# Optimization experiments

Hardware: AMD Instinct MI355X
Metric: run time of the kernel (lower is better)

The kernel has to match this reference:

```python
import jax, jax.numpy as jnp
import numpy as np

B, D, O = 512, 256, 256
H = [512, 1024, 1024]

def _linear_params(key, fan_in, fan_out):
    kw, kb = jax.random.split(key)
    bound = 1.0 / np.sqrt(fan_in)
    W = jax.random.uniform(kw, (fan_out, fan_in), jnp.float32, -bound, bound)
    b = jax.random.uniform(kb, (fan_out,), jnp.float32, -bound, bound)
    return W, b

def setup_inputs() -> dict:
    key = jax.random.key(0)
    ks = jax.random.split(key, 7)
    input_values = jax.random.normal(ks[0], (B, D), jnp.float32)
    nan_flag = jax.random.uniform(ks[1], (B, D), jnp.float32)
    W_in, b_in = _linear_params(ks[2], D, H[0])          # input_layer: nan_flag_dim -> H[0]
    W_h1, b_h1 = _linear_params(ks[3], H[0], H[1])        # hidden layer 1
    W_h2, b_h2 = _linear_params(ks[4], H[1], H[2])        # hidden layer 2
    W_d, b_d = _linear_params(ks[5], H[2], D * O)         # output_branch_dense
    W_b, b_b = _linear_params(ks[6], H[2], O)             # output_branch_bias
    return {"input_values": input_values, "nan_flag": nan_flag, "training": False,
            "W_in": W_in, "b_in": b_in, "W_h1": W_h1, "b_h1": b_h1,
            "W_h2": W_h2, "b_h2": b_h2, "W_d": W_d, "b_d": b_d,
            "W_b": W_b, "b_b": b_b}

def reference(input_values, nan_flag, training, W_in, b_in, W_h1, b_h1, W_h2, b_h2, W_d, b_d, W_b, b_b):
    # training=False: dropout is identity, sample_missing branch skipped (default False)
    x = jax.nn.relu(nan_flag @ W_in.T + b_in)
    x = jax.nn.relu(x @ W_h1.T + b_h1)
    x = jax.nn.relu(x @ W_h2.T + b_h2)
    # per-sample compensation weights [B, D, O] and bias [B, O]
    comp_w = (x @ W_d.T + b_d).reshape(B, D, O)
    comp_b = x @ W_b.T + b_b
    # baddbmm: [B,1,D] @ [B,D,O] + [B,1,O] -> squeeze -> [B,O]
    out = comp_b + jnp.einsum('bd,bdo->bo', input_values, comp_w)
    return out
```

## Files before the change

kernel.cpp:

```cpp
#include <hip/hip_runtime.h>
#include <hip/hip_bf16.h>

#define B_  512
#define D_  256
#define O_  256
#define H2_ 1024

typedef __attribute__((ext_vector_type(4))) float  f32x4;
typedef __attribute__((ext_vector_type(8))) short  short8;
typedef __attribute__((ext_vector_type(4))) short  short4v;

union S8u { short4v v; unsigned u[2]; };

__device__ __forceinline__ unsigned f32_bf16(float x) {
  unsigned u = __builtin_bit_cast(unsigned, x);
  return (u + 0x7fffu + ((u >> 16) & 1u)) >> 16;
}
__device__ __forceinline__ unsigned cvt_pk_bf16(float a, float b) {
  return f32_bf16(a) | (f32_bf16(b) << 16);
}

template <int RELU>
__global__ __launch_bounds__(256)
void gemm_bt64(const float* __restrict__ A, const float* __restrict__ Bm,
               const float* __restrict__ bias, float* __restrict__ C,
               int M, int N, int K) {
  __shared__ __align__(16) short As[64][72];
  __shared__ __align__(16) short Bs[64][72];
  const int t    = threadIdx.x;
  const int m0   = blockIdx.y * 64;
  const int n0   = blockIdx.x * 64;
  const int f4c  = t & 15;
  const int rg   = t >> 4;
  const int lane = t & 63;
  const int w    = t >> 6;
  const int wm   = (w & 1) * 32;
  const int wn   = (w >> 1) * 32;
  const int lr   = lane & 15;
  const int lq   = lane >> 4;

  f32x4 acc[2][2];
  #pragma unroll
  for (int i = 0; i < 2; ++i)
    #pragma unroll
    for (int j = 0; j < 2; ++j) acc[i][j] = f32x4{0.f, 0.f, 0.f, 0.f};

  for (int k0 = 0; k0 < K; k0 += 64) {
    #pragma unroll
    for (int j = 0; j < 4; ++j) {
      int r = rg + 16 * j;
      f32x4 av = *(const f32x4*)(A  + (size_t)(m0 + r) * K + k0 + f4c * 4);
      f32x4 bv = *(const f32x4*)(Bm + (size_t)(n0 + r) * K + k0 + f4c * 4);
      S8u sa; sa.u[0] = cvt_pk_bf16(av.x, av.y); sa.u[1] = cvt_pk_bf16(av.z, av.w);
      S8u sb; sb.u[0] = cvt_pk_bf16(bv.x, bv.y); sb.u[1] = cvt_pk_bf16(bv.z, bv.w);
      *(short4v*)&As[r][f4c * 4] = sa.v;
      *(short4v*)&Bs[r][f4c * 4] = sb.v;
    }
    __syncthreads();
    #pragma unroll
    for (int ks = 0; ks < 2; ++ks) {
      short8 a0 = *(const short8*)&As[wm + lr     ][ks * 32 + lq * 8];
      short8 a1 = *(const short8*)&As[wm + 16 + lr][ks * 32 + lq * 8];
      short8 b0 = *(const short8*)&Bs[wn + lr     ][ks * 32 + lq * 8];
      short8 b1 = *(const short8*)&Bs[wn + 16 + lr][ks * 32 + lq * 8];
      acc[0][0] = __builtin_amdgcn_mfma_f32_16x16x32_bf16(a0, b0, acc[0][0], 0, 0, 0);
      acc[0][1] = __builtin_amdgcn_mfma_f32_16x16x32_bf16(a0, b1, acc[0][1], 0, 0, 0);
      acc[1][0] = __builtin_amdgcn_mfma_f32_16x16x32_bf16(a1, b0, acc[1][0], 0, 0, 0);
      acc[1][1] = __builtin_amdgcn_mfma_f32_16x16x32_bf16(a1, b1, acc[1][1], 0, 0, 0);
    }
    __syncthreads();
  }
  #pragma unroll
  for (int mi = 0; mi < 2; ++mi)
    #pragma unroll
    for (int ni = 0; ni < 2; ++ni)
      #pragma unroll
      for (int r = 0; r < 4; ++r) {
        int row = m0 + wm + mi * 16 + lq * 4 + r;
        int col = n0 + wn + ni * 16 + lr;
        float v = acc[mi][ni][r] + bias[col];
        if (RELU) v = fmaxf(v, 0.f);
        C[(size_t)row * N + col] = v;
      }
}

__global__ __launch_bounds__(256)
void bias_d_kernel(const float* __restrict__ inp, const float* __restrict__ b_d,
                   float* __restrict__ out) {
  const int b = blockIdx.x;
  const int o = threadIdx.x;
  const float* ir = inp + (size_t)b * D_;
  float s = 0.f;
  for (int d = 0; d < D_; ++d)
    s += ir[d] * b_d[(size_t)d * O_ + o];
  out[(size_t)b * O_ + o] += s;
}

__global__ __launch_bounds__(256, 2)
void stage_b(const float* __restrict__ x2, const float* __restrict__ inp,
             const float* __restrict__ Wd, float* __restrict__ out) {
  __shared__ __align__(16) short As[128][72];
  __shared__ __align__(16) short Bs[128][72];
  const int t    = threadIdx.x;
  const int mt   = blockIdx.x >> 1;
  const int nt   = blockIdx.x & 1;
  const int d0   = blockIdx.y * 4;
  const int bm   = mt * 128;
  const int bn   = nt * 128;
  const int f4c  = t & 15;
  const int rg   = t >> 4;
  const int lane = t & 63;
  const int w    = t >> 6;
  const int wm   = (w & 1) * 64;
  const int wn   = (w >> 1) * 64;
  const int lr   = lane & 15;
  const int lq   = lane >> 4;

  f32x4 acc[4][4];
  #pragma unroll
  for (int mi = 0; mi < 4; ++mi)
    #pragma unroll
    for (int ni = 0; ni < 4; ++ni) acc[mi][ni] = f32x4{0.f, 0.f, 0.f, 0.f};

  for (int dl = 0; dl < 4; ++dl) {
    const int d = d0 + dl;
    float insc[8];
    #pragma unroll
    for (int j = 0; j < 8; ++j)
      insc[j] = inp[(size_t)(bm + rg + 16 * j) * D_ + d];
    const float* wbase = Wd + ((size_t)d * O_ + bn) * H2_;

    for (int h0 = 0; h0 < H2_; h0 += 64) {
      #pragma unroll
      for (int j = 0; j < 8; ++j) {
        int r = rg + 16 * j;
        f32x4 xv = *(const f32x4*)(x2 + (size_t)(bm + r) * H2_ + h0 + f4c * 4);
        float s = insc[j];
        S8u sa;
        sa.u[0] = cvt_pk_bf16(xv.x * s, xv.y * s);
        sa.u[1] = cvt_pk_bf16(xv.z * s, xv.w * s);
        *(short4v*)&As[r][f4c * 4] = sa.v;
        f32x4 wv = *(const f32x4*)(wbase + (size_t)r * H2_ + h0 + f4c * 4);
        S8u sb; sb.u[0] = cvt_pk_bf16(wv.x, wv.y); sb.u[1] = cvt_pk_bf16(wv.z, wv.w);
        *(short4v*)&Bs[r][f4c * 4] = sb.v;
      }
      __syncthreads();
      #pragma unroll
      for (int ks = 0; ks < 2; ++ks) {
        short8 af[4], bfr[4];
        #pragma unroll
        for (int mi = 0; mi < 4; ++mi)
          af[mi] = *(const short8*)&As[wm + mi * 16 + lr][ks * 32 + lq * 8];
        #pragma unroll
        for (int ni = 0; ni < 4; ++ni)
          bfr[ni] = *(const short8*)&Bs[wn + ni * 16 + lr][ks * 32 + lq * 8];
        #pragma unroll
        for (int mi = 0; mi < 4; ++mi)
          #pragma unroll
          for (int ni = 0; ni < 4; ++ni)
            acc[mi][ni] = __builtin_amdgcn_mfma_f32_16x16x32_bf16(af[mi], bfr[ni],
                                                                  acc[mi][ni], 0, 0, 0);
      }
      __syncthreads();
    }
  }

  #pragma unroll
  for (int mi = 0; mi < 4; ++mi)
    #pragma unroll
    for (int ni = 0; ni < 4; ++ni)
      #pragma unroll
      for (int r = 0; r < 4; ++r) {
        int row = bm + wm + mi * 16 + lq * 4 + r;
        int col = bn + wn + ni * 16 + lr;
        atomicAdd(out + (size_t)row * O_ + col, acc[mi][ni][r]);
      }
}

extern "C" void kernel_launch(void* const* d_in, const int* in_sizes, int n_in,
                              void* d_out, int out_size, void* d_ws, size_t ws_size,
                              hipStream_t stream) {
  const float* input = (const float*)d_in[0];
  const float* nanf  = (const float*)d_in[1];
  const float* W_in  = (const float*)d_in[3];
  const float* b_in  = (const float*)d_in[4];
  const float* W_h1  = (const float*)d_in[5];
  const float* b_h1  = (const float*)d_in[6];
  const float* W_h2  = (const float*)d_in[7];
  const float* b_h2  = (const float*)d_in[8];
  const float* W_d   = (const float*)d_in[9];
  const float* b_d   = (const float*)d_in[10];
  const float* W_b   = (const float*)d_in[11];
  const float* b_b   = (const float*)d_in[12];
  float* out = (float*)d_out;

  float* x0 = (float*)d_ws;
  float* x1 = x0 + 512 * 512;
  float* x2 = x1 + 512 * 1024;

  gemm_bt64<1><<<dim3(512 / 64, 512 / 64), 256, 0, stream>>>(nanf, W_in, b_in, x0, 512, 512, 256);
  gemm_bt64<1><<<dim3(1024 / 64, 512 / 64), 256, 0, stream>>>(x0, W_h1, b_h1, x1, 512, 1024, 512);
  gemm_bt64<1><<<dim3(1024 / 64, 512 / 64), 256, 0, stream>>>(x1, W_h2, b_h2, x2, 512, 1024, 1024);
  gemm_bt64<0><<<dim3(256 / 64, 512 / 64), 256, 0, stream>>>(x2, W_b, b_b, out, 512, 256, 1024);
  bias_d_kernel<<<512, 256, 0, stream>>>(input, b_d, out);
  stage_b<<<dim3(8, 64), 256, 0, stream>>>(x2, input, W_d, out);
}
```

Baseline: 628.4 us.

## Pre-convert W_d to bf16 and stream it into LDS asynchronously

Adds a conversion kernel that turns the large W_d matrix into bf16 in workspace on every call. A new stage_b2 kernel then loads W_d tiles with global_load_lds straight into a swizzled LDS layout. It processes two d values per block with twice as many blocks and a higher occupancy hint. The aim is to halve the bytes that the four repeated per-M-tile reads of W_d must move and to remove the in-loop conversion, at the cost of an extra full read and write pass over W_d. The bias_d loop is also unrolled.

```diff
diff --git a/kernel.cpp b/kernel.cpp
--- a/kernel.cpp
+++ b/kernel.cpp
@@ -10,7 +10,8 @@
 typedef __attribute__((ext_vector_type(8))) short  short8;
 typedef __attribute__((ext_vector_type(4))) short  short4v;
 
-union S8u { short4v v; unsigned u[2]; };
+union S8u  { short4v v; unsigned u[2]; };
+union S16u { short8  v; unsigned u[4]; };
 
 __device__ __forceinline__ unsigned f32_bf16(float x) {
   unsigned u = __builtin_bit_cast(unsigned, x);
@@ -18,6 +19,28 @@
 }
 __device__ __forceinline__ unsigned cvt_pk_bf16(float a, float b) {
   return f32_bf16(a) | (f32_bf16(b) << 16);
+}
+
+__device__ __forceinline__ void gl_lds16(const void* g, void* l) {
+  __builtin_amdgcn_global_load_lds(
+      (const __attribute__((address_space(1))) unsigned int*)g,
+      (__attribute__((address_space(3))) unsigned int*)l, 16, 0, 0);
+}
+
+__global__ __launch_bounds__(256)
+void wcvt(const float* __restrict__ src, ushort* __restrict__ dst, int n8) {
+  int i = blockIdx.x * 256 + threadIdx.x;
+  const int stride = gridDim.x * 256;
+  for (; i < n8; i += stride) {
+    const f32x4* p = (const f32x4*)(src + (size_t)i * 8);
+    f32x4 a = p[0], b = p[1];
+    S16u s;
+    s.u[0] = cvt_pk_bf16(a.x, a.y);
+    s.u[1] = cvt_pk_bf16(a.z, a.w);
+    s.u[2] = cvt_pk_bf16(b.x, b.y);
+    s.u[3] = cvt_pk_bf16(b.z, b.w);
+    *(short8*)(dst + (size_t)i * 8) = s.v;
+  }
 }
 
 template <int RELU>
@@ -91,9 +114,98 @@
   const int o = threadIdx.x;
   const float* ir = inp + (size_t)b * D_;
   float s = 0.f;
+  #pragma unroll 8
   for (int d = 0; d < D_; ++d)
     s += ir[d] * b_d[(size_t)d * O_ + o];
   out[(size_t)b * O_ + o] += s;
+}
+
+__global__ __launch_bounds__(256, 4)
+void stage_b2(const float* __restrict__ x2, const float* __restrict__ inp,
+              const ushort* __restrict__ Wdb, float* __restrict__ out) {
+  __shared__ __align__(16) short  As[128][72];
+  __shared__ __align__(16) ushort Bs[128 * 64];
+  const int t    = threadIdx.x;
+  const int mt   = blockIdx.x >> 1;
+  const int nt   = blockIdx.x & 1;
+  const int d0   = blockIdx.y * 2;
+  const int bm   = mt * 128;
+  const int bn   = nt * 128;
+  const int f4c  = t & 15;
+  const int rg   = t >> 4;
+  const int lane = t & 63;
+  const int w    = t >> 6;
+  const int wm   = (w & 1) * 64;
+  const int wn   = (w >> 1) * 64;
+  const int lr   = lane & 15;
+  const int lq   = lane >> 4;
+  const int srow = t >> 3;
+  const int skc  = (t & 7) ^ ((t >> 3) & 7);
+
+  f32x4 acc[4][4];
+  #pragma unroll
+  for (int mi = 0; mi < 4; ++mi)
+    #pragma unroll
+    for (int ni = 0; ni < 4; ++ni) acc[mi][ni] = f32x4{0.f, 0.f, 0.f, 0.f};
+
+  for (int dl = 0; dl < 2; ++dl) {
+    const int d = d0 + dl;
+    float insc[8];
+    #pragma unroll
+    for (int j = 0; j < 8; ++j)
+      insc[j] = inp[(size_t)(bm + rg + 16 * j) * D_ + d];
+    const ushort* wb = Wdb + ((size_t)d * O_ + bn) * H2_;
+
+    for (int h0 = 0; h0 < H2_; h0 += 64) {
+      #pragma unroll
+      for (int r = 0; r < 4; ++r) {
+        int n = r * 32 + srow;
+        gl_lds16(wb + (size_t)n * H2_ + h0 + skc * 8, &Bs[(size_t)(r * 256 + t) * 8]);
+      }
+      #pragma unroll
+      for (int j = 0; j < 8; ++j) {
+        int rrow = rg + 16 * j;
+        f32x4 xv = *(const f32x4*)(x2 + (size_t)(bm + rrow) * H2_ + h0 + f4c * 4);
+        float s = insc[j];
+        S8u sa;
+        sa.u[0] = cvt_pk_bf16(xv.x * s, xv.y * s);
+        sa.u[1] = cvt_pk_bf16(xv.z * s, xv.w * s);
+        *(short4v*)&As[rrow][f4c * 4] = sa.v;
+      }
+      __syncthreads();
+      #pragma unroll
+      for (int ks = 0; ks < 2; ++ks) {
+        short8 af[4], bfr[4];
+        #pragma unroll
+        for (int mi = 0; mi < 4; ++mi)
+          af[mi] = *(const short8*)&As[wm + mi * 16 + lr][ks * 32 + lq * 8];
+        #pragma unroll
+        for (int ni = 0; ni < 4; ++ni) {
+          int n  = wn + ni * 16 + lr;
+          int kc = (ks * 4 + lq) ^ (n & 7);
+          bfr[ni] = *(const short8*)&Bs[(size_t)(n * 8 + kc) * 8];
+        }
+        #pragma unroll
+        for (int mi = 0; mi < 4; ++mi)
+          #pragma unroll
+          for (int ni = 0; ni < 4; ++ni)
+            acc[mi][ni] = __builtin_amdgcn_mfma_f32_16x16x32_bf16(af[mi], bfr[ni],
+                                                                  acc[mi][ni], 0, 0, 0);
+      }
+      __syncthreads();
+    }
+  }
+
+  #pragma unroll
+  for (int mi = 0; mi < 4; ++mi)
+    #pragma unroll
+    for (int ni = 0; ni < 4; ++ni)
+      #pragma unroll
+      for (int r = 0; r < 4; ++r) {
+        int row = bm + wm + mi * 16 + lq * 4 + r;
+        int col = bn + wn + ni * 16 + lr;
+        atomicAdd(out + (size_t)row * O_ + col, acc[mi][ni][r]);
+      }
 }
 
 __global__ __launch_bounds__(256, 2)
@@ -197,11 +309,21 @@
   float* x0 = (float*)d_ws;
   float* x1 = x0 + 512 * 512;
   float* x2 = x1 + 512 * 1024;
-
-  gemm_bt64<1><<<dim3(512 / 64, 512 / 64), 256, 0, stream>>>(nanf, W_in, b_in, x0, 512, 512, 256);
-  gemm_bt64<1><<<dim3(1024 / 64, 512 / 64), 256, 0, stream>>>(x0, W_h1, b_h1, x1, 512, 1024, 512);
-  gemm_bt64<1><<<dim3(1024 / 64, 512 / 64), 256, 0, stream>>>(x1, W_h2, b_h2, x2, 512, 1024, 1024);
-  gemm_bt64<0><<<dim3(256 / 64, 512 / 64), 256, 0, stream>>>(x2, W_b, b_b, out, 512, 256, 1024);
+  ushort* Wdb = (ushort*)(x2 + 512 * 1024);
+  const size_t need = 5242880 + (size_t)65536 * 1024 * 2;
+  const bool use_bf16_w = ws_size >= need;
+
+  if (use_bf16_w)
+    wcvt<<<8192, 256, 0, stream>>>(W_d, Wdb, 65536 * 1024 / 8);
+
+  gemm_bt64<1><<<dim3(8, 8),  256, 0, stream>>>(nanf, W_in, b_in, x0, 512, 512, 256);
+  gemm_bt64<1><<<dim3(16, 8), 256, 0, stream>>>(x0, W_h1, b_h1, x1, 512, 1024, 512);
+  gemm_bt64<1><<<dim3(16, 8), 256, 0, stream>>>(x1, W_h2, b_h2, x2, 512, 1024, 1024);
+  gemm_bt64<0><<<dim3(4, 8),  256, 0, stream>>>(x2, W_b, b_b, out, 512, 256, 1024);
   bias_d_kernel<<<512, 256, 0, stream>>>(input, b_d, out);
-  stage_b<<<dim3(8, 64), 256, 0, stream>>>(x2, input, W_d, out);
-}
+
+  if (use_bf16_w)
+    stage_b2<<<dim3(8, 128), 256, 0, stream>>>(x2, input, Wdb, out);
+  else
+    stage_b<<<dim3(8, 64), 256, 0, stream>>>(x2, input, W_d, out);
+}
```

After: 906.5 us. 44.2% more time.
